# Kernel optimization log

Measured on AMD Instinct MI355X. Metric: run time of the kernel, lower is better.

The kernel has to match this reference:

```python
import jax, jax.numpy as jnp
import numpy as np

N, DM, F, G, FG = 4096, 512, 128, 8, 16
DH, DE, ES = 128, 256, 4
E = G * ES
GROUP_TOP_K, EXPERT_TOP_K = 2, 2
TEMP = 1.0
LN_EPS = 1e-5


def _ln(x, g, b):
    m = jnp.mean(x, axis=-1, keepdims=True)
    v = jnp.mean((x - m) ** 2, axis=-1, keepdims=True)
    return (x - m) * jax.lax.rsqrt(v + LN_EPS) * g + b


def _topk_softmax(logits, k):
    # faithful to torch _topk_softmax: softmax over top-k values, zeros elsewhere
    vals, idx = jax.lax.top_k(logits, k)
    w = jax.nn.softmax(vals, axis=-1)
    oh = jax.nn.one_hot(idx, logits.shape[-1], dtype=logits.dtype)  # [..., k, E]
    return jnp.einsum('...ke,...k->...e', oh, w)


def setup_inputs() -> dict:
    key = jax.random.key(0)
    ks = iter(jax.random.split(key, 32))
    n = lambda shape, s=0.02: jax.random.normal(next(ks), shape, dtype=jnp.float32) * s
    d = {
        'hidden': jax.random.normal(next(ks), (N, DM), dtype=jnp.float32),
        'feat': jax.random.normal(next(ks), (N, F), dtype=jnp.float32),
        # pre_ln
        'pre_ln_g': jnp.ones((DM,), jnp.float32), 'pre_ln_b': jnp.zeros((DM,), jnp.float32),
        # router_hidden_encoder: LN(DM) -> Lin(DM,DH) -> GELU -> Lin(DH,DH)
        'rh_ln_g': jnp.ones((DM,), jnp.float32), 'rh_ln_b': jnp.zeros((DM,), jnp.float32),
        'rh_w1': n((DM, DH)), 'rh_b1': jnp.zeros((DH,), jnp.float32),
        'rh_w2': n((DH, DH)), 'rh_b2': jnp.zeros((DH,), jnp.float32),
        # stage_feature_encoder: LN(F) -> Lin(F,DH) -> GELU -> Lin(DH,DH)
        'sf_ln_g': jnp.ones((F,), jnp.float32), 'sf_ln_b': jnp.zeros((F,), jnp.float32),
        'sf_w1': n((F, DH)), 'sf_b1': jnp.zeros((DH,), jnp.float32),
        'sf_w2': n((DH, DH)), 'sf_b2': jnp.zeros((DH,), jnp.float32),
        # group_feature_encoders (stacked over G): LN(FG) -> Lin(FG,DH) -> GELU -> Lin(DH,DH)
        'gf_ln_g': jnp.ones((G, FG), jnp.float32), 'gf_ln_b': jnp.zeros((G, FG), jnp.float32),
        'gf_w1': n((G, FG, DH)), 'gf_b1': jnp.zeros((G, DH), jnp.float32),
        'gf_w2': n((G, DH, DH)), 'gf_b2': jnp.zeros((G, DH), jnp.float32),
        # per_group_scorer (ScalarRouter): Lin(4DH,DH) -> GELU -> Lin(DH,1)
        'pgs_w1': n((4 * DH, DH)), 'pgs_b1': jnp.zeros((DH,), jnp.float32),
        'pgs_w2': n((DH,)), 'pgs_b2': jnp.zeros((), jnp.float32),
        # intra_routers (stacked over G): Lin(4DH,DH) -> GELU -> Lin(DH,ES)
        'ir_w1': n((G, 4 * DH, DH)), 'ir_b1': jnp.zeros((G, DH), jnp.float32),
        'ir_w2': n((G, DH, ES)), 'ir_b2': jnp.zeros((G, ES), jnp.float32),
        # experts (stacked over E = G*ES, group-major): Lin(DM,DE) -> GELU -> Lin(DE,DM)
        'ex_w1': n((E, DM, DE)), 'ex_b1': jnp.zeros((E, DE), jnp.float32),
        'ex_w2': n((E, DE, DM)), 'ex_b2': jnp.zeros((E, DM), jnp.float32),
    }
    return d


def reference(hidden, feat, pre_ln_g, pre_ln_b, rh_ln_g, rh_ln_b, rh_w1, rh_b1, rh_w2, rh_b2,
              sf_ln_g, sf_ln_b, sf_w1, sf_b1, sf_w2, sf_b2,
              gf_ln_g, gf_ln_b, gf_w1, gf_b1, gf_w2, gf_b2,
              pgs_w1, pgs_b1, pgs_w2, pgs_b2,
              ir_w1, ir_b1, ir_w2, ir_b2,
              ex_w1, ex_b1, ex_w2, ex_b2):
    # expert input (pre-LN hidden)
    h_norm = _ln(hidden, pre_ln_g, pre_ln_b)                         # [N, DM]

    # factorized router encoders
    h_enc = jax.nn.gelu(_ln(hidden, rh_ln_g, rh_ln_b) @ rh_w1 + rh_b1) @ rh_w2 + rh_b2   # [N, DH]
    s_enc = jax.nn.gelu(_ln(feat, sf_ln_g, sf_ln_b) @ sf_w1 + sf_b1) @ sf_w2 + sf_b2     # [N, DH]
    gfeat = feat.reshape(N, G, FG)                                    # disjoint contiguous group features
    g_h = jax.nn.gelu(jnp.einsum('ngf,gfh->ngh', _ln(gfeat, gf_ln_g, gf_ln_b), gf_w1) + gf_b1)
    g_enc = jnp.einsum('ngh,ghk->ngk', g_h, gf_w2) + gf_b2            # [N, G, DH]

    hB = jnp.broadcast_to(h_enc[:, None, :], (N, G, DH))
    sB = jnp.broadcast_to(s_enc[:, None, :], (N, G, DH))
    router_in = jnp.concatenate([hB, sB, g_enc, hB * g_enc], axis=-1)  # [N, G, 4DH]

    # per-group scalar scores -> group logits -> top-k scatter softmax
    pg_h = jax.nn.gelu(jnp.einsum('ngi,ih->ngh', router_in, pgs_w1) + pgs_b1)
    group_logits = (jnp.einsum('ngh,h->ng', pg_h, pgs_w2) + pgs_b2) / max(TEMP, 1e-6)    # [N, G]
    group_w = _topk_softmax(group_logits, GROUP_TOP_K)                 # [N, G]

    # intra-group expert routers -> top-k scatter softmax over expert_scale
    ir_h = jax.nn.gelu(jnp.einsum('ngi,gih->ngh', router_in, ir_w1) + ir_b1)
    intra_logits = jnp.einsum('ngh,ghe->nge', ir_h, ir_w2) + ir_b2     # [N, G, ES]
    intra_w = _topk_softmax(intra_logits, EXPERT_TOP_K)                # [N, G, ES]

    comb_w = (group_w[:, :, None] * intra_w).reshape(N, E)             # group-major expert order

    # per-expert GELU MLPs on pre-LN hidden (dense compute, sparse weights)
    eh = jax.nn.gelu(jnp.einsum('nd,edh->neh', h_norm, ex_w1) + ex_b1) # [N, E, DE]
    eo = jnp.einsum('neh,ehd->ned', eh, ex_w2) + ex_b2                 # [N, E, DM]
    out = jnp.einsum('ne,ned->nd', comb_w, eo)                         # [N, DM]
    return out
```

## Files before the change

### kernel.cpp

```cpp
#include <hip/hip_runtime.h>
#include <hip/hip_bf16.h>
#include <math.h>

#define N_TOK 4096
#define DM 512
#define FDIM 128
#define G 8
#define FG 16
#define DH 128
#define DE 256
#define ES 4
#define E_EXP 32
#define LN_EPS 1e-5f
#define BT 32

typedef __attribute__((ext_vector_type(8))) short bf16x8;
typedef __attribute__((ext_vector_type(4))) float f32x4;

#define MFMA16(a, b, c) __builtin_amdgcn_mfma_f32_16x16x32_bf16((a), (b), (c), 0, 0, 0)

__device__ __forceinline__ float gelu_t(float x) {
    const float c = 0.7978845608028654f;
    float x3 = x * x * x;
    return 0.5f * x * (1.0f + tanhf(c * (x + 0.044715f * x3)));
}

__device__ __forceinline__ short f2bf(float f) {
    __hip_bfloat16 h = __float2bfloat16(f);
    return *reinterpret_cast<short*>(&h);
}
__device__ __forceinline__ float bf2f(short s) {
    __hip_bfloat16 h = *reinterpret_cast<__hip_bfloat16*>(&s);
    return __bfloat162float(h);
}
__device__ __forceinline__ void split3(float x, short& h, short& m, short& l) {
    h = f2bf(x);
    float r = x - bf2f(h);
    m = f2bf(r);
    float r2 = r - bf2f(m);
    l = f2bf(r2);
}

__global__ void k_ln_hidden(const float* __restrict__ hidden,
                            const float* __restrict__ pg, const float* __restrict__ pb,
                            const float* __restrict__ rg, const float* __restrict__ rb,
                            __hip_bfloat16* __restrict__ h_normb, float* __restrict__ hL) {
    int n = blockIdx.x;
    int j = threadIdx.x;
    const float* x = hidden + (size_t)n * DM;
    float v0 = x[j], v1 = x[j + 256];
    float s = v0 + v1, q = v0 * v0 + v1 * v1;
#pragma unroll
    for (int o = 32; o; o >>= 1) { s += __shfl_down(s, o); q += __shfl_down(q, o); }
    __shared__ float red[8];
    int w = j >> 6;
    if ((j & 63) == 0) { red[w] = s; red[4 + w] = q; }
    __syncthreads();
    float sum = red[0] + red[1] + red[2] + red[3];
    float sq  = red[4] + red[5] + red[6] + red[7];
    float m = sum * (1.0f / DM);
    float var = sq * (1.0f / DM) - m * m;
    float rs = rsqrtf(var + LN_EPS);
    float t0 = (v0 - m) * rs, t1 = (v1 - m) * rs;
    size_t base = (size_t)n * DM;
    h_normb[base + j]       = __float2bfloat16(t0 * pg[j]       + pb[j]);
    h_normb[base + j + 256] = __float2bfloat16(t1 * pg[j + 256] + pb[j + 256]);
    hL[base + j]           = t0 * rg[j]       + rb[j];
    hL[base + j + 256]     = t1 * rg[j + 256] + rb[j + 256];
}

struct ConvJob { const float* src; short* dh; short* dm; short* dl;
                 int KB, NB, Kreal, plain, blk0; };
struct ConvJobs { ConvJob j[10]; };

__global__ void k_conv_all(ConvJobs J) {
    int b = blockIdx.x;
    int ji = 0;
#pragma unroll
    for (int i = 1; i < 10; i++) if (b >= J.j[i].blk0) ji = i;
    const ConvJob jb = J.j[ji];
    int rel = b - jb.blk0;
    int mat = rel / jb.KB, kb = rel % jb.KB;
    int ncols = jb.NB * 16;
    const float* s = jb.src + (size_t)mat * jb.Kreal * ncols;
    size_t dbase = ((size_t)mat * jb.KB + kb) * jb.NB * 512;
    for (int p = threadIdx.x; p < jb.NB * 64; p += 256) {
        int nb = p >> 6, lane = p & 63;
        int row0 = kb * 32 + ((lane >> 4) << 3);
        int col = nb * 16 + (lane & 15);
        if (jb.plain) {
            union { short sh[8]; uint4 v; } t;
#pragma unroll
            for (int j = 0; j < 8; j++) {
                float x = (row0 + j < jb.Kreal) ? s[(size_t)(row0 + j) * ncols + col] : 0.f;
                t.sh[j] = f2bf(x);
            }
            *(uint4*)&jb.dh[dbase + (size_t)p * 8] = t.v;
        } else {
            union { short sh[8]; uint4 v; } hi, mi, lo;
#pragma unroll
            for (int j = 0; j < 8; j++) {
                float x = (row0 + j < jb.Kreal) ? s[(size_t)(row0 + j) * ncols + col] : 0.f;
                split3(x, hi.sh[j], mi.sh[j], lo.sh[j]);
            }
            *(uint4*)&jb.dh[dbase + (size_t)p * 8] = hi.v;
            *(uint4*)&jb.dm[dbase + (size_t)p * 8] = mi.v;
            *(uint4*)&jb.dl[dbase + (size_t)p * 8] = lo.v;
        }
    }
}

template <int KB_TOT, bool DO_LN>
__device__ __forceinline__ void enc2_body(
        int bx, char* smem,
        const float* __restrict__ X,
        const float* __restrict__ lng, const float* __restrict__ lnb,
        const short* __restrict__ W1h, const short* __restrict__ W1m, const short* __restrict__ W1l,
        const float* __restrict__ B1,
        const short* __restrict__ W2h, const short* __restrict__ W2m, const short* __restrict__ W2l,
        const float* __restrict__ B2,
        float* __restrict__ Y) {
    constexpr int K = KB_TOT * 32;
    const int n0 = bx * 32;
    const int tid = threadIdx.x;
    const int wave = tid >> 6, lane = tid & 63;
    const int quad = lane >> 4, lm = lane & 15;
    const int mt = wave & 1;
    const int ngb = (wave >> 1) * 4;

    short (*Ah)[132] = (short(*)[132])smem;
    short (*Am)[132] = (short(*)[132])(smem + 32 * 132 * 2);
    short (*Al)[132] = (short(*)[132])(smem + 2 * 32 * 132 * 2);

    f32x4 acc[4];
#pragma unroll
    for (int i = 0; i < 4; i++) acc[i] = (f32x4)(0.f);

    if (DO_LN) {
        for (int idx = tid; idx < 1024; idx += 256) {
            int row = idx >> 5, c4 = (idx & 31) * 4;
            float4 v = *(const float4*)&X[(size_t)(n0 + row) * K + c4];
            float s = v.x + v.y + v.z + v.w;
            float q = v.x * v.x + v.y * v.y + v.z * v.z + v.w * v.w;
#pragma unroll
            for (int o = 16; o; o >>= 1) { s += __shfl_xor(s, o); q += __shfl_xor(q, o); }
            float mean = s * (1.0f / 128.0f);
            float var = q * (1.0f / 128.0f) - mean * mean;
            float rs = rsqrtf(var + LN_EPS);
            float xv[4] = {(v.x - mean) * rs * lng[c4 + 0] + lnb[c4 + 0],
                           (v.y - mean) * rs * lng[c4 + 1] + lnb[c4 + 1],
                           (v.z - mean) * rs * lng[c4 + 2] + lnb[c4 + 2],
                           (v.w - mean) * rs * lng[c4 + 3] + lnb[c4 + 3]};
#pragma unroll
            for (int j = 0; j < 4; j++) {
                short h, m, l; split3(xv[j], h, m, l);
                Ah[row][c4 + j] = h; Am[row][c4 + j] = m; Al[row][c4 + j] = l;
            }
        }
        __syncthreads();
#pragma unroll
        for (int kb = 0; kb < KB_TOT; kb++) {
            bf16x8 ah = *(const bf16x8*)&Ah[mt * 16 + lm][kb * 32 + quad * 8];
            bf16x8 am = *(const bf16x8*)&Am[mt * 16 + lm][kb * 32 + quad * 8];
            bf16x8 al = *(const bf16x8*)&Al[mt * 16 + lm][kb * 32 + quad * 8];
#pragma unroll
            for (int nt = 0; nt < 4; nt++) {
                size_t bi = (((size_t)kb * 8 + ngb + nt) * 64 + lane) * 8;
                bf16x8 bh = *(const bf16x8*)&W1h[bi];
                bf16x8 bm = *(const bf16x8*)&W1m[bi];
                bf16x8 bl = *(const bf16x8*)&W1l[bi];
                acc[nt] = MFMA16(al, bh, acc[nt]);
                acc[nt] = MFMA16(am, bm, acc[nt]);
                acc[nt] = MFMA16(ah, bl, acc[nt]);
                acc[nt] = MFMA16(am, bh, acc[nt]);
                acc[nt] = MFMA16(ah, bm, acc[nt]);
                acc[nt] = MFMA16(ah, bh, acc[nt]);
            }
        }
    } else {
        for (int kb = 0; kb < KB_TOT; kb++) {
            const float* xs = X + (size_t)(n0 + mt * 16 + lm) * K + kb * 32 + quad * 8;
            float4 x0 = *(const float4*)xs, x1 = *(const float4*)(xs + 4);
            float xv[8] = {x0.x, x0.y, x0.z, x0.w, x1.x, x1.y, x1.z, x1.w};
            bf16x8 ah, am, al;
#pragma unroll
            for (int j = 0; j < 8; j++) {
                short h, m, l; split3(xv[j], h, m, l);
                ah[j] = h; am[j] = m; al[j] = l;
            }
#pragma unroll
            for (int nt = 0; nt < 4; nt++) {
                size_t bi = (((size_t)kb * 8 + ngb + nt) * 64 + lane) * 8;
                bf16x8 bh = *(const bf16x8*)&W1h[bi];
                bf16x8 bm = *(const bf16x8*)&W1m[bi];
                bf16x8 bl = *(const bf16x8*)&W1l[bi];
                acc[nt] = MFMA16(al, bh, acc[nt]);
                acc[nt] = MFMA16(am, bm, acc[nt]);
                acc[nt] = MFMA16(ah, bl, acc[nt]);
                acc[nt] = MFMA16(am, bh, acc[nt]);
                acc[nt] = MFMA16(ah, bm, acc[nt]);
                acc[nt] = MFMA16(ah, bh, acc[nt]);
            }
        }
    }
    __syncthreads();
#pragma unroll
    for (int nt = 0; nt < 4; nt++) {
        int col = (ngb + nt) * 16 + lm;
        float b1 = B1[col];
#pragma unroll
        for (int r = 0; r < 4; r++) {
            int row = mt * 16 + quad * 4 + r;
            short h, m, l; split3(gelu_t(acc[nt][r] + b1), h, m, l);
            Ah[row][col] = h; Am[row][col] = m; Al[row][col] = l;
        }
    }
    __syncthreads();
    f32x4 acc2[4];
#pragma unroll
    for (int i = 0; i < 4; i++) acc2[i] = (f32x4)(0.f);
#pragma unroll
    for (int kb = 0; kb < 4; kb++) {
        bf16x8 ah = *(const bf16x8*)&Ah[mt * 16 + lm][kb * 32 + quad * 8];
        bf16x8 am = *(const bf16x8*)&Am[mt * 16 + lm][kb * 32 + quad * 8];
        bf16x8 al = *(const bf16x8*)&Al[mt * 16 + lm][kb * 32 + quad * 8];
#pragma unroll
        for (int nt = 0; nt < 4; nt++) {
            size_t bi = (((size_t)kb * 8 + ngb + nt) * 64 + lane) * 8;
            bf16x8 bh = *(const bf16x8*)&W2h[bi];
            bf16x8 bm = *(const bf16x8*)&W2m[bi];
            bf16x8 bl = *(const bf16x8*)&W2l[bi];
            acc2[nt] = MFMA16(al, bh, acc2[nt]);
            acc2[nt] = MFMA16(am, bm, acc2[nt]);
            acc2[nt] = MFMA16(ah, bl, acc2[nt]);
            acc2[nt] = MFMA16(am, bh, acc2[nt]);
            acc2[nt] = MFMA16(ah, bm, acc2[nt]);
            acc2[nt] = MFMA16(ah, bh, acc2[nt]);
        }
    }
#pragma unroll
    for (int nt = 0; nt < 4; nt++) {
        int col = (ngb + nt) * 16 + lm;
        float b2 = B2[col];
#pragma unroll
        for (int r = 0; r < 4; r++) {
            int row = mt * 16 + quad * 4 + r;
            Y[(size_t)(n0 + row) * DH + col] = acc2[nt][r] + b2;
        }
    }
}

__device__ __forceinline__ void genc_one(
        int bx, int g, char* smem,
        const float* __restrict__ feat,
        const float* __restrict__ gln_g, const float* __restrict__ gln_b,
        const short* __restrict__ W1h, const short* __restrict__ W1m, const short* __restrict__ W1l,
        const float* __restrict__ gb1,
        const short* __restrict__ W2h, const short* __restrict__ W2m, const short* __restrict__ W2l,
        const float* __restrict__ gb2,
        float* __restrict__ g_enc) {
    const int n0 = bx * 32;
    const int tid = threadIdx.x;
    const int wave = tid >> 6, lane = tid & 63;
    const int quad = lane >> 4, lm = lane & 15;
    const int mt = wave & 1;
    const int ngb = (wave >> 1) * 4;

    short (*Ah)[132] = (short(*)[132])smem;
    short (*Am)[132] = (short(*)[132])(smem + 8448);
    short (*Al)[132] = (short(*)[132])(smem + 2 * 8448);

    {
        int t = tid >> 3, sub = tid & 7;
        const float* fr = feat + (size_t)(n0 + t) * FDIM + g * FG;
        float xv[FG];
        float mean = 0.f;
#pragma unroll
        for (int i = 0; i < FG; i++) { xv[i] = fr[i]; mean += xv[i]; }
        mean *= (1.0f / FG);
        float var = 0.f;
#pragma unroll
        for (int i = 0; i < FG; i++) { float d = xv[i] - mean; var += d * d; }
        var *= (1.0f / FG);
        float rs = rsqrtf(var + LN_EPS);
#pragma unroll
        for (int j = 0; j < 2; j++) {
            int i = sub * 2 + j;
            float xn = (xv[i] - mean) * rs * gln_g[g * FG + i] + gln_b[g * FG + i];
            short h, m, l; split3(xn, h, m, l);
            Ah[t][i] = h; Am[t][i] = m; Al[t][i] = l;
            Ah[t][16 + i] = 0; Am[t][16 + i] = 0; Al[t][16 + i] = 0;
        }
    }
    __syncthreads();
    f32x4 acc[4];
#pragma unroll
    for (int i = 0; i < 4; i++) acc[i] = (f32x4)(0.f);
    {
        bf16x8 ah = *(const bf16x8*)&Ah[mt * 16 + lm][quad * 8];
        bf16x8 am = *(const bf16x8*)&Am[mt * 16 + lm][quad * 8];
        bf16x8 al = *(const bf16x8*)&Al[mt * 16 + lm][quad * 8];
#pragma unroll
        for (int nt = 0; nt < 4; nt++) {
            size_t bi = (((size_t)g * 8 + ngb + nt) * 64 + lane) * 8;
            bf16x8 bh = *(const bf16x8*)&W1h[bi];
            bf16x8 bm = *(const bf16x8*)&W1m[bi];
            bf16x8 bl = *(const bf16x8*)&W1l[bi];
            acc[nt] = MFMA16(al, bh, acc[nt]);
            acc[nt] = MFMA16(am, bm, acc[nt]);
            acc[nt] = MFMA16(ah, bl, acc[nt]);
            acc[nt] = MFMA16(am, bh, acc[nt]);
            acc[nt] = MFMA16(ah, bm, acc[nt]);
            acc[nt] = MFMA16(ah, bh, acc[nt]);
        }
    }
    __syncthreads();
#pragma unroll
    for (int nt = 0; nt < 4; nt++) {
        int col = (ngb + nt) * 16 + lm;
        float b1 = gb1[g * DH + col];
#pragma unroll
        for (int r = 0; r < 4; r++) {
            int row = mt * 16 + quad * 4 + r;
            short h, m, l; split3(gelu_t(acc[nt][r] + b1), h, m, l);
            Ah[row][col] = h; Am[row][col] = m; Al[row][col] = l;
        }
    }
    __syncthreads();
    f32x4 acc2[4];
#pragma unroll
    for (int i = 0; i < 4; i++) acc2[i] = (f32x4)(0.f);
#pragma unroll
    for (int kb = 0; kb < 4; kb++) {
        bf16x8 a2h = *(const bf16x8*)&Ah[mt * 16 + lm][kb * 32 + quad * 8];
        bf16x8 a2m = *(const bf16x8*)&Am[mt * 16 + lm][kb * 32 + quad * 8];
        bf16x8 a2l = *(const bf16x8*)&Al[mt * 16 + lm][kb * 32 + quad * 8];
#pragma unroll
        for (int nt = 0; nt < 4; nt++) {
            size_t bi = ((((size_t)g * 4 + kb) * 8 + ngb + nt) * 64 + lane) * 8;
            bf16x8 bh = *(const bf16x8*)&W2h[bi];
            bf16x8 bm = *(const bf16x8*)&W2m[bi];
            bf16x8 bl = *(const bf16x8*)&W2l[bi];
            acc2[nt] = MFMA16(a2l, bh, acc2[nt]);
            acc2[nt] = MFMA16(a2m, bm, acc2[nt]);
            acc2[nt] = MFMA16(a2h, bl, acc2[nt]);
            acc2[nt] = MFMA16(a2m, bh, acc2[nt]);
            acc2[nt] = MFMA16(a2h, bm, acc2[nt]);
            acc2[nt] = MFMA16(a2h, bh, acc2[nt]);
        }
    }
#pragma unroll
    for (int nt = 0; nt < 4; nt++) {
        int col = (ngb + nt) * 16 + lm;
        float b2 = gb2[g * DH + col];
#pragma unroll
        for (int r = 0; r < 4; r++) {
            int row = mt * 16 + quad * 4 + r;
            g_enc[((size_t)(n0 + row) * G + g) * DH + col] = acc2[nt][r] + b2;
        }
    }
}

__global__ __launch_bounds__(256) void k_enc_all(
        const float* __restrict__ hL, const float* __restrict__ feat,
        const float* __restrict__ sf_g, const float* __restrict__ sf_b,
        const float* __restrict__ gln_g, const float* __restrict__ gln_b,
        const short* Brh1H, const short* Brh1M, const short* Brh1L, const float* rh_b1,
        const short* Brh2H, const short* Brh2M, const short* Brh2L, const float* rh_b2,
        const short* Bsf1H, const short* Bsf1M, const short* Bsf1L, const float* sf_b1,
        const short* Bsf2H, const short* Bsf2M, const short* Bsf2L, const float* sf_b2,
        const short* Bgf1H, const short* Bgf1M, const short* Bgf1L, const float* gf_b1,
        const short* Bgf2H, const short* Bgf2M, const short* Bgf2L, const float* gf_b2,
        float* __restrict__ h_enc, float* __restrict__ s_enc, float* __restrict__ g_enc) {
    __shared__ __align__(16) char smem[3 * 8448];
    int bid = blockIdx.x;
    if (bid < 128)
        enc2_body<16, false>(bid, smem, hL, nullptr, nullptr,
                             Brh1H, Brh1M, Brh1L, rh_b1, Brh2H, Brh2M, Brh2L, rh_b2, h_enc);
    else if (bid < 256)
        enc2_body<4, true>(bid - 128, smem, feat, sf_g, sf_b,
                           Bsf1H, Bsf1M, Bsf1L, sf_b1, Bsf2H, Bsf2M, Bsf2L, sf_b2, s_enc);
    else {
        int idx = bid - 256;
        genc_one(idx >> 3, idx & 7, smem, feat, gln_g, gln_b,
                 Bgf1H, Bgf1M, Bgf1L, gf_b1, Bgf2H, Bgf2M, Bgf2L, gf_b2, g_enc);
    }
}

__global__ void k_stage_hs(const float* __restrict__ h_enc, const float* __restrict__ s_enc,
                           short* __restrict__ Ah, short* __restrict__ Am, short* __restrict__ Al) {
    int T16 = blockIdx.x;
    for (int slot = threadIdx.x; slot < 512; slot += 256) {
        int kb = slot >> 6, lane = slot & 63;
        int quad = lane >> 4, lm = lane & 15;
        int n = T16 * 16 + lm;
        int c0 = kb * 32 + quad * 8;
        const float* src = (c0 < 128) ? (h_enc + (size_t)n * DH + c0)
                                      : (s_enc + (size_t)n * DH + (c0 - 128));
        float4 x0 = *(const float4*)src;
        float4 x1 = *(const float4*)(src + 4);
        float xv[8] = {x0.x, x0.y, x0.z, x0.w, x1.x, x1.y, x1.z, x1.w};
        union { short sh[8]; uint4 v; } hi, mi, lo;
#pragma unroll
        for (int j = 0; j < 8; j++) split3(xv[j], hi.sh[j], mi.sh[j], lo.sh[j]);
        size_t base = ((size_t)T16 * 512 + slot) * 8;
        *(uint4*)&Ah[base] = hi.v;
        *(uint4*)&Am[base] = mi.v;
        *(uint4*)&Al[base] = lo.v;
    }
}

__global__ __launch_bounds__(512) void k_router_mfma(
        const short* __restrict__ AhsH, const short* __restrict__ AhsM, const short* __restrict__ AhsL,
        const float* __restrict__ h_enc, const float* __restrict__ g_enc,
        const short* __restrict__ BpgH, const short* __restrict__ BpgM, const short* __restrict__ BpgL,
        const short* __restrict__ BirH, const short* __restrict__ BirM, const short* __restrict__ BirL,
        const float* __restrict__ pb1, const float* __restrict__ pw2, const float* __restrict__ pb2,
        const float* __restrict__ ib1, const float* __restrict__ iw2, const float* __restrict__ ib2,
        float* __restrict__ glog, float* __restrict__ ilog) {
    const int g = blockIdx.x & 7;
    const int bx = blockIdx.x >> 3;
    const int n0 = bx * 64;
    const int tid = threadIdx.x;
    const int wave = tid >> 6, lane = tid & 63;
    const int quad = lane >> 4, lm = lane & 15;
    const bool is_pg = wave < 4;
    const int nbase = (wave & 3) * 2;
    const short* Bh = is_pg ? BpgH : (BirH + (size_t)g * 65536);
    const short* Bm = is_pg ? BpgM : (BirM + (size_t)g * 65536);
    const short* Bl = is_pg ? BpgL : (BirL + (size_t)g * 65536);

    __shared__ __align__(16) char smem[49152];

    f32x4 acc[4][2];
#pragma unroll
    for (int mt = 0; mt < 4; mt++)
#pragma unroll
        for (int nt = 0; nt < 2; nt++) acc[mt][nt] = (f32x4)(0.f);

    for (int ch = 0; ch < 4; ch++) {
        __syncthreads();
        for (int idx = tid; idx < 1024; idx += 512) {
            int kbl = idx >> 8, rem = idx & 255;
            int t16 = rem >> 6, lane2 = rem & 63;
            int gkb = ch * 4 + kbl;
            size_t loff = (size_t)kbl * 4096 + t16 * 1024 + (size_t)lane2 * 16;
            if (gkb < 8) {
                int T16g = bx * 4 + t16;
                size_t ai = (((size_t)T16g * 8 + gkb) * 64 + lane2) * 8;
                *(uint4*)(smem + loff)         = *(const uint4*)&AhsH[ai];
                *(uint4*)(smem + 16384 + loff) = *(const uint4*)&AhsM[ai];
                *(uint4*)(smem + 32768 + loff) = *(const uint4*)&AhsL[ai];
            } else {
                int n = n0 + t16 * 16 + (lane2 & 15);
                int c0 = (gkb - 8) * 32 + (lane2 >> 4) * 8;
                float xv[8];
                if (c0 < 128) {
                    const float* gs = g_enc + ((size_t)n * G + g) * DH + c0;
                    float4 x0 = *(const float4*)gs, x1 = *(const float4*)(gs + 4);
                    xv[0]=x0.x; xv[1]=x0.y; xv[2]=x0.z; xv[3]=x0.w;
                    xv[4]=x1.x; xv[5]=x1.y; xv[6]=x1.z; xv[7]=x1.w;
                } else {
                    int c = c0 - 128;
                    const float* gs = g_enc + ((size_t)n * G + g) * DH + c;
                    const float* hsrc = h_enc + (size_t)n * DH + c;
                    float4 g0 = *(const float4*)gs, g1 = *(const float4*)(gs + 4);
                    float4 h0 = *(const float4*)hsrc, h1 = *(const float4*)(hsrc + 4);
                    xv[0]=h0.x*g0.x; xv[1]=h0.y*g0.y; xv[2]=h0.z*g0.z; xv[3]=h0.w*g0.w;
                    xv[4]=h1.x*g1.x; xv[5]=h1.y*g1.y; xv[6]=h1.z*g1.z; xv[7]=h1.w*g1.w;
                }
                union { short sh[8]; uint4 v; } hi, mi, lo;
#pragma unroll
                for (int j = 0; j < 8; j++) split3(xv[j], hi.sh[j], mi.sh[j], lo.sh[j]);
                *(uint4*)(smem + loff)         = hi.v;
                *(uint4*)(smem + 16384 + loff) = mi.v;
                *(uint4*)(smem + 32768 + loff) = lo.v;
            }
        }
        __syncthreads();
#pragma unroll
        for (int kbl = 0; kbl < 4; kbl++) {
            int kb = ch * 4 + kbl;
            bf16x8 Ahf[4], Amf[4], Alf[4];
#pragma unroll
            for (int mt = 0; mt < 4; mt++) {
                size_t loff = (size_t)kbl * 4096 + mt * 1024 + (size_t)lane * 16;
                Ahf[mt] = *(const bf16x8*)(smem + loff);
                Amf[mt] = *(const bf16x8*)(smem + 16384 + loff);
                Alf[mt] = *(const bf16x8*)(smem + 32768 + loff);
            }
#pragma unroll
            for (int nt = 0; nt < 2; nt++) {
                int nb = nbase + nt;
                size_t bi = (((size_t)kb * 8 + nb) * 64 + lane) * 8;
                bf16x8 bh = *(const bf16x8*)&Bh[bi];
                bf16x8 bm = *(const bf16x8*)&Bm[bi];
                bf16x8 bl = *(const bf16x8*)&Bl[bi];
#pragma unroll
                for (int mt = 0; mt < 4; mt++) {
                    acc[mt][nt] = MFMA16(Alf[mt], bh, acc[mt][nt]);
                    acc[mt][nt] = MFMA16(Amf[mt], bm, acc[mt][nt]);
                    acc[mt][nt] = MFMA16(Ahf[mt], bl, acc[mt][nt]);
                    acc[mt][nt] = MFMA16(Amf[mt], bh, acc[mt][nt]);
                    acc[mt][nt] = MFMA16(Ahf[mt], bm, acc[mt][nt]);
                    acc[mt][nt] = MFMA16(Ahf[mt], bh, acc[mt][nt]);
                }
            }
        }
    }

    float (*ph)[129] = (float(*)[129])smem;
    float (*ih)[129] = (float(*)[129])(smem + 32 * 129 * 4);
    for (int h = 0; h < 2; h++) {
        __syncthreads();
#pragma unroll
        for (int mi = 0; mi < 2; mi++) {
            int mt = 2 * h + mi;
#pragma unroll
            for (int nt = 0; nt < 2; nt++) {
                int col = (nbase + nt) * 16 + lm;
                float b1 = is_pg ? pb1[col] : ib1[g * DH + col];
                float* dst = is_pg ? &ph[0][0] : &ih[0][0];
#pragma unroll
                for (int r = 0; r < 4; r++) {
                    int row = mi * 16 + quad * 4 + r;
                    dst[row * 129 + col] = gelu_t(acc[mt][nt][r] + b1);
                }
            }
        }
        __syncthreads();
        if (tid < 32) {
            float s = pb2[0];
            for (int i = 0; i < DH; i++) s += ph[tid][i] * pw2[i];
            glog[(size_t)(n0 + h * 32 + tid) * G + g] = s;
        } else if (tid >= 128 && tid < 256) {
            int t = (tid - 128) >> 2, e = (tid - 128) & 3;
            float s = ib2[g * ES + e];
            const float* w = iw2 + (size_t)g * DH * ES;
            for (int i = 0; i < DH; i++) s += ih[t][i] * w[i * ES + e];
            ilog[((size_t)(n0 + h * 32 + t) * G + g) * ES + e] = s;
        }
    }
}

__global__ void k_topk(const float* __restrict__ glog, const float* __restrict__ ilog,
                       int* __restrict__ cnt, int* __restrict__ toks, float* __restrict__ wgts) {
    int n = blockIdx.x * blockDim.x + threadIdx.x;
    if (n >= N_TOK) return;
    float gl[G];
#pragma unroll
    for (int g = 0; g < G; g++) gl[g] = glog[(size_t)n * G + g];
    int i1 = 0; float v1 = gl[0];
#pragma unroll
    for (int g = 1; g < G; g++) if (gl[g] > v1) { v1 = gl[g]; i1 = g; }
    int i2 = -1; float v2 = -1e30f;
#pragma unroll
    for (int g = 0; g < G; g++) if (g != i1 && gl[g] > v2) { v2 = gl[g]; i2 = g; }
    float eg = expf(v2 - v1);
    float den = 1.0f / (1.0f + eg);
    float gw_sel[2] = { den, eg * den };
    int g_sel[2] = { i1, i2 };
#pragma unroll
    for (int s = 0; s < 2; s++) {
        int g = g_sel[s]; float gw = gw_sel[s];
        float il[ES];
#pragma unroll
        for (int e = 0; e < ES; e++) il[e] = ilog[((size_t)n * G + g) * ES + e];
        int j1 = 0; float u1 = il[0];
#pragma unroll
        for (int e = 1; e < ES; e++) if (il[e] > u1) { u1 = il[e]; j1 = e; }
        int j2 = -1; float u2 = -1e30f;
#pragma unroll
        for (int e = 0; e < ES; e++) if (e != j1 && il[e] > u2) { u2 = il[e]; j2 = e; }
        float ei = expf(u2 - u1);
        float d2 = 1.0f / (1.0f + ei);
        int ex1 = g * ES + j1, ex2 = g * ES + j2;
        int p1 = atomicAdd(&cnt[ex1], 1);
        toks[(size_t)ex1 * N_TOK + p1] = n * 4 + s * 2;     wgts[(size_t)ex1 * N_TOK + p1] = gw * d2;
        int p2 = atomicAdd(&cnt[ex2], 1);
        toks[(size_t)ex2 * N_TOK + p2] = n * 4 + s * 2 + 1; wgts[(size_t)ex2 * N_TOK + p2] = gw * ei * d2;
    }
}

__global__ __launch_bounds__(512) void k_expert_mfma(
        const __hip_bfloat16* __restrict__ h_normb,
        const short* __restrict__ wB1, const float* __restrict__ eb1,
        const short* __restrict__ wB2, const float* __restrict__ eb2,
        const int* __restrict__ cnt, const int* __restrict__ toks,
        const float* __restrict__ wgts, float* __restrict__ part) {
    const int e = blockIdx.x & 31;
    const int slot = blockIdx.x >> 5;
    const int c = cnt[e];
    const int start = slot * BT;
    if (start >= c) return;
    const int m = min(BT, c - start);

    __shared__ short hs[BT][520];
    __shared__ short es[BT][264];
    __shared__ int   tok_s[BT];
    __shared__ float w_s[BT];

    const int tid = threadIdx.x;
    if (tid < BT) {
        bool ok = tid < m;
        tok_s[tid] = ok ? toks[(size_t)e * N_TOK + start + tid] : 0;
        w_s[tid]   = ok ? wgts[(size_t)e * N_TOK + start + tid] : 0.f;
    }
    __syncthreads();
    for (int idx = tid; idx < BT * 64; idx += 512) {
        int t = idx >> 6, ch = idx & 63;
        uint4 v = make_uint4(0, 0, 0, 0);
        if (t < m) v = *((const uint4*)(h_normb + (size_t)(tok_s[t] >> 2) * DM) + ch);
        *(uint4*)&hs[t][ch * 8] = v;
    }
    __syncthreads();

    const int wave = tid >> 6, lane = tid & 63;
    const int quad = lane >> 4, lm = lane & 15;

    {
        const int ng = wave * 2;
        f32x4 acc[2][2];
#pragma unroll
        for (int a = 0; a < 2; a++)
#pragma unroll
            for (int b = 0; b < 2; b++) acc[a][b] = (f32x4)(0.f);
        const short* w1e = wB1 + (size_t)e * DM * DE;
        for (int kb = 0; kb < 16; kb++) {
            bf16x8 a0 = *(const bf16x8*)&hs[lm][kb * 32 + quad * 8];
            bf16x8 a1 = *(const bf16x8*)&hs[16 + lm][kb * 32 + quad * 8];
            const short* wp = w1e + ((size_t)kb * 16 + ng) * 512 + lane * 8;
#pragma unroll
            for (int nt = 0; nt < 2; nt++) {
                bf16x8 b = *(const bf16x8*)(wp + nt * 512);
                acc[0][nt] = MFMA16(a0, b, acc[0][nt]);
                acc[1][nt] = MFMA16(a1, b, acc[1][nt]);
            }
        }
#pragma unroll
        for (int nt = 0; nt < 2; nt++) {
            int col = (ng + nt) * 16 + lm;
            float b1 = eb1[e * DE + col];
#pragma unroll
            for (int mt = 0; mt < 2; mt++)
#pragma unroll
            for (int r = 0; r < 4; r++) {
                int row = mt * 16 + quad * 4 + r;
                es[row][col] = f2bf(gelu_t(acc[mt][nt][r] + b1));
            }
        }
    }
    __syncthreads();

    {
        const int ng2 = wave * 4;
        f32x4 acc[2][4];
#pragma unroll
        for (int a = 0; a < 2; a++)
#pragma unroll
            for (int b = 0; b < 4; b++) acc[a][b] = (f32x4)(0.f);
        const short* w2e = wB2 + (size_t)e * DE * DM;
        for (int kb = 0; kb < 8; kb++) {
            bf16x8 a0 = *(const bf16x8*)&es[lm][kb * 32 + quad * 8];
            bf16x8 a1 = *(const bf16x8*)&es[16 + lm][kb * 32 + quad * 8];
            const short* wp = w2e + ((size_t)kb * 32 + ng2) * 512 + lane * 8;
#pragma unroll
            for (int nt = 0; nt < 4; nt++) {
                bf16x8 b = *(const bf16x8*)(wp + nt * 512);
                acc[0][nt] = MFMA16(a0, b, acc[0][nt]);
                acc[1][nt] = MFMA16(a1, b, acc[1][nt]);
            }
        }
        const float* b2 = eb2 + (size_t)e * DM;
#pragma unroll
        for (int mt = 0; mt < 2; mt++)
#pragma unroll
        for (int r = 0; r < 4; r++) {
            int row = mt * 16 + quad * 4 + r;
            if (row < m) {
                float w = w_s[row];
                float* prow = part + (size_t)tok_s[row] * DM;
#pragma unroll
                for (int nt = 0; nt < 4; nt++) {
                    int col = (ng2 + nt) * 16 + lm;
                    prow[col] = w * (acc[mt][nt][r] + b2[col]);
                }
            }
        }
    }
}

__global__ void k_reduce(const float* __restrict__ part, float* __restrict__ out) {
    int n = blockIdx.x;
    int j = threadIdx.x;
    const float4* p = (const float4*)(part + (size_t)n * 4 * DM);
    float4 a = p[j], b = p[128 + j], c = p[256 + j], d = p[384 + j];
    float4 r = make_float4(a.x + b.x + c.x + d.x, a.y + b.y + c.y + d.y,
                           a.z + b.z + c.z + d.z, a.w + b.w + c.w + d.w);
    ((float4*)(out + (size_t)n * DM))[j] = r;
}

extern "C" void kernel_launch(void* const* d_in, const int* in_sizes, int n_in,
                              void* d_out, int out_size, void* d_ws, size_t ws_size,
                              hipStream_t stream) {
    const float* hidden  = (const float*)d_in[0];
    const float* feat    = (const float*)d_in[1];
    const float* pre_g   = (const float*)d_in[2];
    const float* pre_b   = (const float*)d_in[3];
    const float* rh_g    = (const float*)d_in[4];
    const float* rh_b    = (const float*)d_in[5];
    const float* rh_w1   = (const float*)d_in[6];
    const float* rh_b1   = (const float*)d_in[7];
    const float* rh_w2   = (const float*)d_in[8];
    const float* rh_b2   = (const float*)d_in[9];
    const float* sf_g    = (const float*)d_in[10];
    const float* sf_b    = (const float*)d_in[11];
    const float* sf_w1   = (const float*)d_in[12];
    const float* sf_b1   = (const float*)d_in[13];
    const float* sf_w2   = (const float*)d_in[14];
    const float* sf_b2   = (const float*)d_in[15];
    const float* gln_g   = (const float*)d_in[16];
    const float* gln_b   = (const float*)d_in[17];
    const float* gf_w1   = (const float*)d_in[18];
    const float* gf_b1   = (const float*)d_in[19];
    const float* gf_w2   = (const float*)d_in[20];
    const float* gf_b2   = (const float*)d_in[21];
    const float* pgs_w1  = (const float*)d_in[22];
    const float* pgs_b1  = (const float*)d_in[23];
    const float* pgs_w2  = (const float*)d_in[24];
    const float* pgs_b2  = (const float*)d_in[25];
    const float* ir_w1   = (const float*)d_in[26];
    const float* ir_b1   = (const float*)d_in[27];
    const float* ir_w2   = (const float*)d_in[28];
    const float* ir_b2   = (const float*)d_in[29];
    const float* ex_w1   = (const float*)d_in[30];
    const float* ex_b1   = (const float*)d_in[31];
    const float* ex_w2   = (const float*)d_in[32];
    const float* ex_b2   = (const float*)d_in[33];
    float* out = (float*)d_out;

    char* w = (char*)d_ws;
    auto alloc = [&](size_t bytes) { void* r = (void*)w; w += (bytes + 255) & ~(size_t)255; return r; };
    __hip_bfloat16* h_normb = (__hip_bfloat16*)alloc((size_t)N_TOK * DM * 2);
    float* h_enc = (float*)alloc((size_t)N_TOK * DH * 4);
    float* s_enc = (float*)alloc((size_t)N_TOK * DH * 4);
    float* g_enc = (float*)alloc((size_t)N_TOK * G * DH * 4);
    float* glog  = (float*)alloc((size_t)N_TOK * G * 4);
    float* ilog  = (float*)alloc((size_t)N_TOK * G * ES * 4);
    float* wgts  = (float*)alloc((size_t)E_EXP * N_TOK * 4);
    short* wB1   = (short*)alloc((size_t)E_EXP * DM * DE * 2);
    short* wB2   = (short*)alloc((size_t)E_EXP * DE * DM * 2);
    short* AhsH  = (short*)alloc((size_t)N_TOK * 256 * 2);
    short* AhsM  = (short*)alloc((size_t)N_TOK * 256 * 2);
    short* AhsL  = (short*)alloc((size_t)N_TOK * 256 * 2);
    short* BpgH  = (short*)alloc((size_t)16 * 8 * 512 * 2);
    short* BpgM  = (short*)alloc((size_t)16 * 8 * 512 * 2);
    short* BpgL  = (short*)alloc((size_t)16 * 8 * 512 * 2);
    short* BirH  = (short*)alloc((size_t)G * 16 * 8 * 512 * 2);
    short* BirM  = (short*)alloc((size_t)G * 16 * 8 * 512 * 2);
    short* BirL  = (short*)alloc((size_t)G * 16 * 8 * 512 * 2);
    short* Brh1H = (short*)alloc((size_t)16 * 8 * 512 * 2);
    short* Brh1M = (short*)alloc((size_t)16 * 8 * 512 * 2);
    short* Brh1L = (short*)alloc((size_t)16 * 8 * 512 * 2);
    short* Brh2H = (short*)alloc((size_t)4 * 8 * 512 * 2);
    short* Brh2M = (short*)alloc((size_t)4 * 8 * 512 * 2);
    short* Brh2L = (short*)alloc((size_t)4 * 8 * 512 * 2);
    short* Bsf1H = (short*)alloc((size_t)4 * 8 * 512 * 2);
    short* Bsf1M = (short*)alloc((size_t)4 * 8 * 512 * 2);
    short* Bsf1L = (short*)alloc((size_t)4 * 8 * 512 * 2);
    short* Bsf2H = (short*)alloc((size_t)4 * 8 * 512 * 2);
    short* Bsf2M = (short*)alloc((size_t)4 * 8 * 512 * 2);
    short* Bsf2L = (short*)alloc((size_t)4 * 8 * 512 * 2);
    short* Bgf1H = (short*)alloc((size_t)G * 1 * 8 * 512 * 2);
    short* Bgf1M = (short*)alloc((size_t)G * 1 * 8 * 512 * 2);
    short* Bgf1L = (short*)alloc((size_t)G * 1 * 8 * 512 * 2);
    short* Bgf2H = (short*)alloc((size_t)G * 4 * 8 * 512 * 2);
    short* Bgf2M = (short*)alloc((size_t)G * 4 * 8 * 512 * 2);
    short* Bgf2L = (short*)alloc((size_t)G * 4 * 8 * 512 * 2);
    int* cnt     = (int*)alloc(E_EXP * 4);
    int* toks    = (int*)alloc((size_t)E_EXP * N_TOK * 4);
    char* uni   = (char*)alloc((size_t)N_TOK * 4 * DM * 4);
    float* hL   = (float*)uni;
    float* part = (float*)uni;

    hipMemsetAsync(cnt, 0, E_EXP * sizeof(int), stream);

    ConvJobs J;
    int b0 = 0;
    auto mkjob = [&](int i, const float* s, short* dh, short* dm, short* dl,
                     int KB, int NB, int Kreal, int plain, int nmat) {
        J.j[i] = ConvJob{s, dh, dm, dl, KB, NB, Kreal, plain, b0};
        b0 += KB * nmat;
    };
    mkjob(0, ex_w1, wB1, nullptr, nullptr, 16, 16, 512, 1, E_EXP);
    mkjob(1, ex_w2, wB2, nullptr, nullptr, 8, 32, 256, 1, E_EXP);
    mkjob(2, pgs_w1, BpgH, BpgM, BpgL, 16, 8, 512, 0, 1);
    mkjob(3, ir_w1, BirH, BirM, BirL, 16, 8, 512, 0, G);
    mkjob(4, rh_w1, Brh1H, Brh1M, Brh1L, 16, 8, 512, 0, 1);
    mkjob(5, rh_w2, Brh2H, Brh2M, Brh2L, 4, 8, 128, 0, 1);
    mkjob(6, sf_w1, Bsf1H, Bsf1M, Bsf1L, 4, 8, 128, 0, 1);
    mkjob(7, sf_w2, Bsf2H, Bsf2M, Bsf2L, 4, 8, 128, 0, 1);
    mkjob(8, gf_w1, Bgf1H, Bgf1M, Bgf1L, 1, 8, 16, 0, G);
    mkjob(9, gf_w2, Bgf2H, Bgf2M, Bgf2L, 4, 8, 128, 0, G);
    k_conv_all<<<b0, 256, 0, stream>>>(J);

    k_ln_hidden<<<N_TOK, 256, 0, stream>>>(hidden, pre_g, pre_b, rh_g, rh_b, h_normb, hL);

    k_enc_all<<<256 + (N_TOK / 32) * G, 256, 0, stream>>>(
        hL, feat, sf_g, sf_b, gln_g, gln_b,
        Brh1H, Brh1M, Brh1L, rh_b1, Brh2H, Brh2M, Brh2L, rh_b2,
        Bsf1H, Bsf1M, Bsf1L, sf_b1, Bsf2H, Bsf2M, Bsf2L, sf_b2,
        Bgf1H, Bgf1M, Bgf1L, gf_b1, Bgf2H, Bgf2M, Bgf2L, gf_b2,
        h_enc, s_enc, g_enc);

    k_stage_hs<<<N_TOK / 16, 256, 0, stream>>>(h_enc, s_enc, AhsH, AhsM, AhsL);

    k_router_mfma<<<(N_TOK / 64) * G, 512, 0, stream>>>(AhsH, AhsM, AhsL, h_enc, g_enc,
                                             BpgH, BpgM, BpgL, BirH, BirM, BirL,
                                             pgs_b1, pgs_w2, pgs_b2, ir_b1, ir_w2, ir_b2,
                                             glog, ilog);

    k_topk<<<N_TOK / 256, 256, 0, stream>>>(glog, ilog, cnt, toks, wgts);
    k_expert_mfma<<<(N_TOK / BT) * E_EXP, 512, 0, stream>>>(h_normb, wB1, ex_b1, wB2, ex_b2,
                                                            cnt, toks, wgts, part);
    k_reduce<<<N_TOK, 128, 0, stream>>>(part, out);
}
```

Baseline: 335.8 us.

## Fuse LN into conversion kernel, inline hs staging into router, alias expert smem

Merges the hidden layernorm kernel into the weight-conversion kernel as extra blocks, which removes one launch. Removes the separate h/s staging kernel, so the router now loads h_enc/s_enc directly and does the three-way bf16 split in-kernel. This drops one launch and the intermediate global buffers, at the cost of repeating the split work once per group block (8x). The expert kernel reuses the hs shared buffer for the GELU intermediate, with an added barrier, to cut LDS use and possibly raise occupancy.

```diff
diff --git a/kernel.cpp b/kernel.cpp
--- a/kernel.cpp
+++ b/kernel.cpp
@@ -41,40 +41,41 @@
     l = f2bf(r2);
 }
 
-__global__ void k_ln_hidden(const float* __restrict__ hidden,
-                            const float* __restrict__ pg, const float* __restrict__ pb,
-                            const float* __restrict__ rg, const float* __restrict__ rb,
-                            __hip_bfloat16* __restrict__ h_normb, float* __restrict__ hL) {
-    int n = blockIdx.x;
-    int j = threadIdx.x;
-    const float* x = hidden + (size_t)n * DM;
-    float v0 = x[j], v1 = x[j + 256];
-    float s = v0 + v1, q = v0 * v0 + v1 * v1;
-#pragma unroll
-    for (int o = 32; o; o >>= 1) { s += __shfl_down(s, o); q += __shfl_down(q, o); }
-    __shared__ float red[8];
-    int w = j >> 6;
-    if ((j & 63) == 0) { red[w] = s; red[4 + w] = q; }
-    __syncthreads();
-    float sum = red[0] + red[1] + red[2] + red[3];
-    float sq  = red[4] + red[5] + red[6] + red[7];
-    float m = sum * (1.0f / DM);
-    float var = sq * (1.0f / DM) - m * m;
-    float rs = rsqrtf(var + LN_EPS);
-    float t0 = (v0 - m) * rs, t1 = (v1 - m) * rs;
-    size_t base = (size_t)n * DM;
-    h_normb[base + j]       = __float2bfloat16(t0 * pg[j]       + pb[j]);
-    h_normb[base + j + 256] = __float2bfloat16(t1 * pg[j + 256] + pb[j + 256]);
-    hL[base + j]           = t0 * rg[j]       + rb[j];
-    hL[base + j + 256]     = t1 * rg[j + 256] + rb[j + 256];
-}
-
 struct ConvJob { const float* src; short* dh; short* dm; short* dl;
                  int KB, NB, Kreal, plain, blk0; };
 struct ConvJobs { ConvJob j[10]; };
 
-__global__ void k_conv_all(ConvJobs J) {
+__global__ void k_pre(ConvJobs J, int nconv,
+                      const float* __restrict__ hidden,
+                      const float* __restrict__ pg, const float* __restrict__ pb,
+                      const float* __restrict__ rg, const float* __restrict__ rb,
+                      __hip_bfloat16* __restrict__ h_normb, float* __restrict__ hL) {
     int b = blockIdx.x;
+    if (b >= nconv) {
+        int n = b - nconv;
+        int j = threadIdx.x;
+        const float* x = hidden + (size_t)n * DM;
+        float v0 = x[j], v1 = x[j + 256];
+        float s = v0 + v1, q = v0 * v0 + v1 * v1;
+#pragma unroll
+        for (int o = 32; o; o >>= 1) { s += __shfl_down(s, o); q += __shfl_down(q, o); }
+        __shared__ float red[8];
+        int w = j >> 6;
+        if ((j & 63) == 0) { red[w] = s; red[4 + w] = q; }
+        __syncthreads();
+        float sum = red[0] + red[1] + red[2] + red[3];
+        float sq  = red[4] + red[5] + red[6] + red[7];
+        float m = sum * (1.0f / DM);
+        float var = sq * (1.0f / DM) - m * m;
+        float rs = rsqrtf(var + LN_EPS);
+        float t0 = (v0 - m) * rs, t1 = (v1 - m) * rs;
+        size_t base = (size_t)n * DM;
+        h_normb[base + j]       = __float2bfloat16(t0 * pg[j]       + pb[j]);
+        h_normb[base + j + 256] = __float2bfloat16(t1 * pg[j + 256] + pb[j + 256]);
+        hL[base + j]           = t0 * rg[j]       + rb[j];
+        hL[base + j + 256]     = t1 * rg[j + 256] + rb[j + 256];
+        return;
+    }
     int ji = 0;
 #pragma unroll
     for (int i = 1; i < 10; i++) if (b >= J.j[i].blk0) ji = i;
@@ -387,32 +388,9 @@
     }
 }
 
-__global__ void k_stage_hs(const float* __restrict__ h_enc, const float* __restrict__ s_enc,
-                           short* __restrict__ Ah, short* __restrict__ Am, short* __restrict__ Al) {
-    int T16 = blockIdx.x;
-    for (int slot = threadIdx.x; slot < 512; slot += 256) {
-        int kb = slot >> 6, lane = slot & 63;
-        int quad = lane >> 4, lm = lane & 15;
-        int n = T16 * 16 + lm;
-        int c0 = kb * 32 + quad * 8;
-        const float* src = (c0 < 128) ? (h_enc + (size_t)n * DH + c0)
-                                      : (s_enc + (size_t)n * DH + (c0 - 128));
-        float4 x0 = *(const float4*)src;
-        float4 x1 = *(const float4*)(src + 4);
-        float xv[8] = {x0.x, x0.y, x0.z, x0.w, x1.x, x1.y, x1.z, x1.w};
-        union { short sh[8]; uint4 v; } hi, mi, lo;
-#pragma unroll
-        for (int j = 0; j < 8; j++) split3(xv[j], hi.sh[j], mi.sh[j], lo.sh[j]);
-        size_t base = ((size_t)T16 * 512 + slot) * 8;
-        *(uint4*)&Ah[base] = hi.v;
-        *(uint4*)&Am[base] = mi.v;
-        *(uint4*)&Al[base] = lo.v;
-    }
-}
-
 __global__ __launch_bounds__(512) void k_router_mfma(
-        const short* __restrict__ AhsH, const short* __restrict__ AhsM, const short* __restrict__ AhsL,
-        const float* __restrict__ h_enc, const float* __restrict__ g_enc,
+        const float* __restrict__ h_enc, const float* __restrict__ s_enc,
+        const float* __restrict__ g_enc,
         const short* __restrict__ BpgH, const short* __restrict__ BpgM, const short* __restrict__ BpgL,
         const short* __restrict__ BirH, const short* __restrict__ BirM, const short* __restrict__ BirL,
         const float* __restrict__ pb1, const float* __restrict__ pw2, const float* __restrict__ pb2,
@@ -445,16 +423,18 @@
             int t16 = rem >> 6, lane2 = rem & 63;
             int gkb = ch * 4 + kbl;
             size_t loff = (size_t)kbl * 4096 + t16 * 1024 + (size_t)lane2 * 16;
+            int n = n0 + t16 * 16 + (lane2 & 15);
+            int csub = (lane2 >> 4) * 8;
+            float xv[8];
             if (gkb < 8) {
-                int T16g = bx * 4 + t16;
-                size_t ai = (((size_t)T16g * 8 + gkb) * 64 + lane2) * 8;
-                *(uint4*)(smem + loff)         = *(const uint4*)&AhsH[ai];
-                *(uint4*)(smem + 16384 + loff) = *(const uint4*)&AhsM[ai];
-                *(uint4*)(smem + 32768 + loff) = *(const uint4*)&AhsL[ai];
+                int c0 = gkb * 32 + csub;
+                const float* src = (c0 < 128) ? (h_enc + (size_t)n * DH + c0)
+                                              : (s_enc + (size_t)n * DH + (c0 - 128));
+                float4 x0 = *(const float4*)src, x1 = *(const float4*)(src + 4);
+                xv[0]=x0.x; xv[1]=x0.y; xv[2]=x0.z; xv[3]=x0.w;
+                xv[4]=x1.x; xv[5]=x1.y; xv[6]=x1.z; xv[7]=x1.w;
             } else {
-                int n = n0 + t16 * 16 + (lane2 & 15);
-                int c0 = (gkb - 8) * 32 + (lane2 >> 4) * 8;
-                float xv[8];
+                int c0 = (gkb - 8) * 32 + csub;
                 if (c0 < 128) {
                     const float* gs = g_enc + ((size_t)n * G + g) * DH + c0;
                     float4 x0 = *(const float4*)gs, x1 = *(const float4*)(gs + 4);
@@ -469,13 +449,13 @@
                     xv[0]=h0.x*g0.x; xv[1]=h0.y*g0.y; xv[2]=h0.z*g0.z; xv[3]=h0.w*g0.w;
                     xv[4]=h1.x*g1.x; xv[5]=h1.y*g1.y; xv[6]=h1.z*g1.z; xv[7]=h1.w*g1.w;
                 }
-                union { short sh[8]; uint4 v; } hi, mi, lo;
-#pragma unroll
-                for (int j = 0; j < 8; j++) split3(xv[j], hi.sh[j], mi.sh[j], lo.sh[j]);
-                *(uint4*)(smem + loff)         = hi.v;
-                *(uint4*)(smem + 16384 + loff) = mi.v;
-                *(uint4*)(smem + 32768 + loff) = lo.v;
-            }
+            }
+            union { short sh[8]; uint4 v; } hi, mi, lo;
+#pragma unroll
+            for (int j = 0; j < 8; j++) split3(xv[j], hi.sh[j], mi.sh[j], lo.sh[j]);
+            *(uint4*)(smem + loff)         = hi.v;
+            *(uint4*)(smem + 16384 + loff) = mi.v;
+            *(uint4*)(smem + 32768 + loff) = lo.v;
         }
         __syncthreads();
 #pragma unroll
@@ -596,7 +576,7 @@
     const int m = min(BT, c - start);
 
     __shared__ short hs[BT][520];
-    __shared__ short es[BT][264];
+    short (*es)[264] = (short(*)[264])&hs[0][0];
     __shared__ int   tok_s[BT];
     __shared__ float w_s[BT];
 
@@ -618,13 +598,13 @@
     const int wave = tid >> 6, lane = tid & 63;
     const int quad = lane >> 4, lm = lane & 15;
 
+    const int ng = wave * 2;
+    f32x4 acc1[2][2];
+#pragma unroll
+    for (int a = 0; a < 2; a++)
+#pragma unroll
+        for (int b = 0; b < 2; b++) acc1[a][b] = (f32x4)(0.f);
     {
-        const int ng = wave * 2;
-        f32x4 acc[2][2];
-#pragma unroll
-        for (int a = 0; a < 2; a++)
-#pragma unroll
-            for (int b = 0; b < 2; b++) acc[a][b] = (f32x4)(0.f);
         const short* w1e = wB1 + (size_t)e * DM * DE;
         for (int kb = 0; kb < 16; kb++) {
             bf16x8 a0 = *(const bf16x8*)&hs[lm][kb * 32 + quad * 8];
@@ -633,21 +613,22 @@
 #pragma unroll
             for (int nt = 0; nt < 2; nt++) {
                 bf16x8 b = *(const bf16x8*)(wp + nt * 512);
-                acc[0][nt] = MFMA16(a0, b, acc[0][nt]);
-                acc[1][nt] = MFMA16(a1, b, acc[1][nt]);
-            }
-        }
-#pragma unroll
-        for (int nt = 0; nt < 2; nt++) {
-            int col = (ng + nt) * 16 + lm;
-            float b1 = eb1[e * DE + col];
-#pragma unroll
-            for (int mt = 0; mt < 2; mt++)
-#pragma unroll
-            for (int r = 0; r < 4; r++) {
-                int row = mt * 16 + quad * 4 + r;
-                es[row][col] = f2bf(gelu_t(acc[mt][nt][r] + b1));
-            }
+                acc1[0][nt] = MFMA16(a0, b, acc1[0][nt]);
+                acc1[1][nt] = MFMA16(a1, b, acc1[1][nt]);
+            }
+        }
+    }
+    __syncthreads();
+#pragma unroll
+    for (int nt = 0; nt < 2; nt++) {
+        int col = (ng + nt) * 16 + lm;
+        float b1 = eb1[e * DE + col];
+#pragma unroll
+        for (int mt = 0; mt < 2; mt++)
+#pragma unroll
+        for (int r = 0; r < 4; r++) {
+            int row = mt * 16 + quad * 4 + r;
+            es[row][col] = f2bf(gelu_t(acc1[mt][nt][r] + b1));
         }
     }
     __syncthreads();
@@ -750,9 +731,6 @@
     float* wgts  = (float*)alloc((size_t)E_EXP * N_TOK * 4);
     short* wB1   = (short*)alloc((size_t)E_EXP * DM * DE * 2);
     short* wB2   = (short*)alloc((size_t)E_EXP * DE * DM * 2);
-    short* AhsH  = (short*)alloc((size_t)N_TOK * 256 * 2);
-    short* AhsM  = (short*)alloc((size_t)N_TOK * 256 * 2);
-    short* AhsL  = (short*)alloc((size_t)N_TOK * 256 * 2);
     short* BpgH  = (short*)alloc((size_t)16 * 8 * 512 * 2);
     short* BpgM  = (short*)alloc((size_t)16 * 8 * 512 * 2);
     short* BpgL  = (short*)alloc((size_t)16 * 8 * 512 * 2);
@@ -802,9 +780,7 @@
     mkjob(7, sf_w2, Bsf2H, Bsf2M, Bsf2L, 4, 8, 128, 0, 1);
     mkjob(8, gf_w1, Bgf1H, Bgf1M, Bgf1L, 1, 8, 16, 0, G);
     mkjob(9, gf_w2, Bgf2H, Bgf2M, Bgf2L, 4, 8, 128, 0, G);
-    k_conv_all<<<b0, 256, 0, stream>>>(J);
-
-    k_ln_hidden<<<N_TOK, 256, 0, stream>>>(hidden, pre_g, pre_b, rh_g, rh_b, h_normb, hL);
+    k_pre<<<b0 + N_TOK, 256, 0, stream>>>(J, b0, hidden, pre_g, pre_b, rh_g, rh_b, h_normb, hL);
 
     k_enc_all<<<256 + (N_TOK / 32) * G, 256, 0, stream>>>(
         hL, feat, sf_g, sf_b, gln_g, gln_b,
@@ -813,9 +789,7 @@
         Bgf1H, Bgf1M, Bgf1L, gf_b1, Bgf2H, Bgf2M, Bgf2L, gf_b2,
         h_enc, s_enc, g_enc);
 
-    k_stage_hs<<<N_TOK / 16, 256, 0, stream>>>(h_enc, s_enc, AhsH, AhsM, AhsL);
-
-    k_router_mfma<<<(N_TOK / 64) * G, 512, 0, stream>>>(AhsH, AhsM, AhsL, h_enc, g_enc,
+    k_router_mfma<<<(N_TOK / 64) * G, 512, 0, stream>>>(h_enc, s_enc, g_enc,
                                              BpgH, BpgM, BpgL, BirH, BirM, BirL,
                                              pgs_b1, pgs_w2, pgs_b2, ir_b1, ir_w2, ir_b2,
                                              glog, ilog);
```

Measured after the change: 320.7 us. -4.5%, faster.
